# Optimization experiments

Hardware: AMD Instinct MI355X
Metric: run time of the kernel (lower is better)

## Reference

```python
import jax, jax.numpy as jnp
import numpy as np

N_CHARS = 50257
CHAR = 512
HID = 1024
LENGTH = 2048


def setup_inputs() -> dict:
    key = jax.random.key(0)
    ks = jax.random.split(key, 8)
    s = 1.0 / np.sqrt(HID)
    sh = 1.0 / np.sqrt(HID)
    return {
        "inputs": jax.random.normal(ks[0], (HID,), jnp.float32),
        "embed": (jax.random.normal(ks[1], (N_CHARS, CHAR), jnp.float32) * 0.02),
        "W_ih": jax.random.uniform(ks[2], (4 * HID, CHAR), jnp.float32, -s, s),
        "W_hh": jax.random.uniform(ks[3], (4 * HID, HID), jnp.float32, -s, s),
        "b_ih": jax.random.uniform(ks[4], (4 * HID,), jnp.float32, -s, s),
        "b_hh": jax.random.uniform(ks[5], (4 * HID,), jnp.float32, -s, s),
        "W_head": jax.random.uniform(ks[6], (N_CHARS, HID), jnp.float32, -sh, sh),
        "b_head": jax.random.uniform(ks[7], (N_CHARS,), jnp.float32, -sh, sh),
        "length": LENGTH,
        "start": 5,
    }


def _lstm_cell(x, h, c, W_ih, W_hh, b_ih, b_hh):
    # PyTorch gate order: i, f, g, o
    gates = W_ih @ x + b_ih + W_hh @ h + b_hh  # [4H]
    i, f, g, o = jnp.split(gates, 4)
    i = jax.nn.sigmoid(i)
    f = jax.nn.sigmoid(f)
    g = jnp.tanh(g)
    o = jax.nn.sigmoid(o)
    c = f * c + i * g
    h = o * jnp.tanh(c)
    return h, c


def reference(inputs, embed, W_ih, W_hh, b_ih, b_hh, W_head, b_head, length, start):
    h0 = inputs                       # latent used as initial hidden state
    c0 = jnp.zeros_like(inputs)
    x0 = embed[start]                 # [CHAR]

    def step(carry, _):
        h, c, x = carry
        h, c = _lstm_cell(x, h, c, W_ih, W_hh, b_ih, b_hh)
        logits = W_head @ h + b_head  # [N_CHARS]
        char = jnp.argmax(logits)
        x = embed[char]
        return (h, c, x), (char, logits)

    _, (chars, logits) = jax.lax.scan(step, (h0, c0, x0), None, length=length)
    return chars, logits
```

## Files before the change

### kernel.cpp

```cpp
#include <hip/hip_runtime.h>
#include <stdint.h>
#include <math.h>

#define HID   1024
#define CHARD 512
#define NC    50257
#define TLEN  2048
#define NBLK  256
#define NTHR  512
#define NGRP2 2048
#define GR    25
#define GRREG 6
#define GRLDS 19
#define NBH   1571
#define SQ    4064.0f
#define INVSQ (1.0f/4064.0f)
#define QERR  (0.5f/4064.0f)
#define CANDR 192
#define FLAGSTRIDE 16

typedef unsigned long long ull;
typedef unsigned char u8;
typedef float f32x4 __attribute__((ext_vector_type(4)));

__device__ __forceinline__ unsigned ford(float f) {
    unsigned b = __float_as_uint(f);
    return (b & 0x80000000u) ? ~b : (b | 0x80000000u);
}
__device__ __forceinline__ float unford(unsigned u) {
    return __uint_as_float((u & 0x80000000u) ? (u & 0x7FFFFFFFu) : ~u);
}
__device__ __forceinline__ ull packkv(float v, unsigned j) {
    return ((ull)ford(v) << 32) | (ull)(0xFFFFFFFFu - j);
}
__device__ __forceinline__ ull umaxu(ull a, ull b) { return a > b ? a : b; }
__device__ __forceinline__ ull shflx_ull(ull v, int m) {
    unsigned lo = (unsigned)v, hi = (unsigned)(v >> 32);
    lo = __shfl_xor(lo, m);
    hi = __shfl_xor(hi, m);
    return ((ull)hi << 32) | lo;
}

#define ALOADF(p)    __hip_atomic_load((p), __ATOMIC_RELAXED, __HIP_MEMORY_SCOPE_AGENT)
#define ASTORE(p, v) __hip_atomic_store((p), (v), __ATOMIC_RELAXED, __HIP_MEMORY_SCOPE_AGENT)

__global__ __launch_bounds__(256) void k_init(const float* __restrict__ inputs,
                                              float* __restrict__ hh,
                                              float* __restrict__ c,
                                              unsigned* __restrict__ flagarea)
{
    int g = blockIdx.x * 256 + threadIdx.x;
    if (g < HID) { hh[g] = inputs[g]; c[g] = 0.f; }
    for (int i = g; i < 2 * NBLK * FLAGSTRIDE + 16; i += 2048) flagarea[i] = 0u;
}

__global__ __launch_bounds__(256) void k_quant(const float* __restrict__ W,
                                               u8* __restrict__ W8)
{
    size_t base = ((size_t)blockIdx.x * 256 + threadIdx.x) * 16;
    if (base >= (size_t)NC * HID) return;
    const float4* src = (const float4*)(W + base);
    uint out[4];
    #pragma unroll
    for (int g = 0; g < 4; ++g) {
        float4 w = src[g];
        int a0 = (__float2int_rn(w.x * SQ) + 128) & 255;
        int a1 = (__float2int_rn(w.y * SQ) + 128) & 255;
        int a2 = (__float2int_rn(w.z * SQ) + 128) & 255;
        int a3 = (__float2int_rn(w.w * SQ) + 128) & 255;
        out[g] = (uint)(a0 | (a1 << 8) | (a2 << 16) | (a3 << 24));
    }
    *(uint4*)(W8 + base) = make_uint4(out[0], out[1], out[2], out[3]);
}

__device__ __forceinline__ float exact_logit(const float4* hs4,
                                             const float* __restrict__ W_head,
                                             const float* __restrict__ b_head,
                                             int j, int lane)
{
    const float4* wr = (const float4*)(W_head + (size_t)j * HID);
    float a = 0.f;
    #pragma unroll
    for (int m = 0; m < 4; ++m) {
        float4 w = wr[m * 64 + lane], v = hs4[m * 64 + lane];
        a = fmaf(w.x, v.x, a); a = fmaf(w.y, v.y, a);
        a = fmaf(w.z, v.z, a); a = fmaf(w.w, v.w, a);
    }
    #pragma unroll
    for (int off = 32; off > 0; off >>= 1) a += __shfl_xor(a, off);
    return a + b_head[j];
}

__device__ __forceinline__ unsigned resolve_char(const float4* hs4,
                                                 ull* bm, float* abuf,
                                                 const float* __restrict__ W_head,
                                                 const float* __restrict__ b_head,
                                                 float Sh, ull* red8, int tid)
{
    __shared__ int s_cnt, s_gcnt;
    __shared__ int s_grps[32];
    __shared__ int s_rows[CANDR];

    const int wave = tid >> 6;
    const int lane = tid & 63;

    ull bmv[4];
    ull pm = 0ull;
    #pragma unroll
    for (int rep = 0; rep < NGRP2 / NTHR; ++rep) {
        bmv[rep] = ALOADF(&bm[tid + rep * NTHR]);
        pm = umaxu(pm, bmv[rep]);
    }
    #pragma unroll
    for (int off = 32; off > 0; off >>= 1) pm = umaxu(pm, shflx_ull(pm, off));
    if (lane == 0) red8[wave] = pm;
    if (tid == 0) { s_cnt = 0; s_gcnt = 0; }
    __syncthreads();
    pm = red8[0];
    #pragma unroll
    for (int w = 1; w < 8; ++w) pm = umaxu(pm, red8[w]);
    const float mtil = unford((unsigned)(pm >> 32));
    const float E = QERR * Sh * 1.02f + 1e-4f;
    const float thresh = mtil - 2.0f * E;
    const ull pkth = ((ull)ford(thresh)) << 32;

    #pragma unroll
    for (int rep = 0; rep < NGRP2 / NTHR; ++rep) {
        if (bmv[rep] >= pkth) {
            int p = atomicAdd(&s_gcnt, 1);
            if (p < 32) s_grps[p] = tid + rep * NTHR;
        }
    }
    __syncthreads();
    const int ngr = s_gcnt;
    int ncr;
    if (ngr <= 32) {
        for (int gq = 0; gq < ngr; ++gq) {
            const int j = s_grps[gq] * GR + tid;
            if (tid < GR && j < NC) {
                float av = ALOADF(&abuf[j]);
                if (av >= thresh) {
                    int p = atomicAdd(&s_cnt, 1);
                    if (p < CANDR) s_rows[p] = j;
                }
            }
        }
        __syncthreads();
        ncr = s_cnt;
    } else {
        ncr = CANDR + 1;
    }

    ull best = 0ull;
    if (ncr <= CANDR) {
        for (int q = wave; q < ncr; q += 8) {
            const int j = s_rows[q];
            best = umaxu(best, packkv(exact_logit(hs4, W_head, b_head, j, lane),
                                      (unsigned)j));
        }
    } else {
        for (int i = wave; i < NGRP2; i += 8) {
            ull bv = ALOADF(&bm[i]);
            if (bv >= pkth) {
                const int jb = i * GR;
                const int je = jb + GR < NC ? jb + GR : NC;
                for (int j = jb; j < je; ++j) {
                    float av = ALOADF(&abuf[j]);
                    if (av >= thresh)
                        best = umaxu(best, packkv(exact_logit(hs4, W_head, b_head, j, lane),
                                                  (unsigned)j));
                }
            }
        }
    }
    __syncthreads();
    if (lane == 0) red8[wave] = best;
    __syncthreads();
    best = red8[0];
    #pragma unroll
    for (int w = 1; w < 8; ++w) best = umaxu(best, red8[w]);
    unsigned idx = 0xFFFFFFFFu - (unsigned)(best & 0xFFFFFFFFull);
    return idx < NC ? idx : (NC - 1);
}

__device__ __forceinline__ float dot16u(uint4 q, float4 h0, float4 h1,
                                        float4 h2, float4 h3)
{
    float a = 0.f;
    a = fmaf((float)(q.x & 255u), h0.x, a);
    a = fmaf((float)((q.x >> 8) & 255u), h0.y, a);
    a = fmaf((float)((q.x >> 16) & 255u), h0.z, a);
    a = fmaf((float)(q.x >> 24), h0.w, a);
    a = fmaf((float)(q.y & 255u), h1.x, a);
    a = fmaf((float)((q.y >> 8) & 255u), h1.y, a);
    a = fmaf((float)((q.y >> 16) & 255u), h1.z, a);
    a = fmaf((float)(q.y >> 24), h1.w, a);
    a = fmaf((float)(q.z & 255u), h2.x, a);
    a = fmaf((float)((q.z >> 8) & 255u), h2.y, a);
    a = fmaf((float)((q.z >> 16) & 255u), h2.z, a);
    a = fmaf((float)(q.z >> 24), h2.w, a);
    a = fmaf((float)(q.w & 255u), h3.x, a);
    a = fmaf((float)((q.w >> 8) & 255u), h3.y, a);
    a = fmaf((float)((q.w >> 16) & 255u), h3.z, a);
    a = fmaf((float)(q.w >> 24), h3.w, a);
    return a;
}

__global__ __launch_bounds__(NTHR, 1) void k_persist(
    const float* __restrict__ W_ih, const float* __restrict__ W_hh,
    const float* __restrict__ b_ih, const float* __restrict__ b_hh,
    const float* __restrict__ embed,
    const float* __restrict__ W_head, const float* __restrict__ b_head,
    const u8* __restrict__ W8,
    float* hh, float* abuf, ull* bm,
    float* __restrict__ chars_out, const int* __restrict__ startp,
    unsigned* flags, unsigned* gen)
{
    __shared__ uint4  w8L[8][GRLDS][64];
    __shared__ float4 hs4[HID / 4];
    __shared__ float4 xs4[CHARD / 4];
    __shared__ ull    red8[8];
    __shared__ float  sred[8], sred2[8];
    __shared__ int    s_brk;

    const int b    = blockIdx.x;
    const int tid  = threadIdx.x;
    const int wave = tid >> 6;
    const int lane = tid & 63;
    const int rL   = b * 4 + wave;
    const int g    = b * 8 + wave;
    const int jb   = g * GR;
    const u8* Wp   = W8 + (size_t)jb * HID;

    uint4 qb[GRREG];
    #pragma unroll
    for (int rr = 0; rr < GRREG; ++rr) {
        const int j = jb + rr;
        qb[rr] = (j < NC) ? ((const uint4*)(Wp + (size_t)rr * HID))[lane]
                          : make_uint4(0, 0, 0, 0);
    }
    #pragma unroll
    for (int rr = 0; rr < GRLDS; ++rr) {
        const int j = jb + GRREG + rr;
        w8L[wave][rr][lane] = (j < NC)
            ? ((const uint4*)(Wp + (size_t)(GRREG + rr) * HID))[lane]
            : make_uint4(0, 0, 0, 0);
    }

    float bsum[4] = {0.f, 0.f, 0.f, 0.f};
    if (wave < 4) {
        #pragma unroll
        for (int q = 0; q < 4; ++q) bsum[q] = b_ih[q * HID + rL] + b_hh[q * HID + rL];
    }
    if (tid == 0) s_brk = 0;
    float creg = 0.f;
    __syncthreads();

    float Sh;
    {
        float sa = 0.f;
        if (tid < 256) {
            float4 hv = ((const float4*)hh)[tid];
            hs4[tid] = hv;
            sa = fabsf(hv.x) + fabsf(hv.y) + fabsf(hv.z) + fabsf(hv.w);
        }
        #pragma unroll
        for (int off = 32; off > 0; off >>= 1) sa += __shfl_xor(sa, off);
        if (lane == 0) sred[wave] = sa;
        __syncthreads();
        Sh = 0.f;
        #pragma unroll
        for (int w = 0; w < 8; ++w) Sh += sred[w];
    }

    unsigned bk = 0;

    #define GRIDBAR()                                                              \
    do {                                                                           \
        ++bk;                                                                      \
        __syncthreads();                                                           \
        if (b == 0) {                                                              \
            if (!s_brk && tid > 0 && tid < NBLK) {                                 \
                int guard = 0;                                                     \
                while (__hip_atomic_load(&flags[tid * FLAGSTRIDE],                 \
                         __ATOMIC_RELAXED, __HIP_MEMORY_SCOPE_AGENT) < bk) {       \
                    __builtin_amdgcn_s_sleep(1);                                   \
                    if (++guard > (1 << 24)) { s_brk = 1; break; }                 \
                }                                                                  \
            }                                                                      \
            __syncthreads();                                                       \
            if (tid < NBLK)                                                        \
                __hip_atomic_store(&gen[tid * FLAGSTRIDE], bk, __ATOMIC_RELAXED,   \
                                   __HIP_MEMORY_SCOPE_AGENT);                      \
        } else {                                                                   \
            if (tid == 0) {                                                        \
                __hip_atomic_store(&flags[b * FLAGSTRIDE], bk, __ATOMIC_RELAXED,   \
                                   __HIP_MEMORY_SCOPE_AGENT);                      \
                if (!s_brk) {                                                      \
                    int guard = 0;                                                 \
                    while (__hip_atomic_load(&gen[b * FLAGSTRIDE],                 \
                             __ATOMIC_RELAXED, __HIP_MEMORY_SCOPE_AGENT) < bk) {   \
                        __builtin_amdgcn_s_sleep(1);                               \
                        if (++guard > (1 << 24)) { s_brk = 1; break; }             \
                    }                                                              \
                }                                                                  \
            }                                                                      \
            __syncthreads();                                                       \
        }                                                                          \
    } while (0)

    for (int t = 0; t < TLEN; ++t) {
        unsigned idx;
        if (t == 0) {
            idx = (unsigned)startp[0];
        } else {
            idx = resolve_char(hs4, bm, abuf, W_head, b_head, Sh, red8, tid);
            if (b == 0 && tid == 0) chars_out[t - 1] = (float)idx;
        }
        if (tid < 128) xs4[tid] = ((const float4*)(embed + (size_t)idx * CHARD))[tid];
        __syncthreads();

        if (wave < 4) {
            float acc[4];
            #pragma unroll
            for (int q = 0; q < 4; ++q) {
                const float4* wi = (const float4*)(W_ih + (size_t)(q * HID + rL) * CHARD);
                const float4* wh = (const float4*)(W_hh + (size_t)(q * HID + rL) * HID);
                float a = 0.f;
                #pragma unroll
                for (int m = 0; m < 2; ++m) {
                    float4 w = wi[m * 64 + lane], v = xs4[m * 64 + lane];
                    a = fmaf(w.x, v.x, a); a = fmaf(w.y, v.y, a);
                    a = fmaf(w.z, v.z, a); a = fmaf(w.w, v.w, a);
                }
                #pragma unroll
                for (int m = 0; m < 4; ++m) {
                    float4 w = wh[m * 64 + lane], v = hs4[m * 64 + lane];
                    a = fmaf(w.x, v.x, a); a = fmaf(w.y, v.y, a);
                    a = fmaf(w.z, v.z, a); a = fmaf(w.w, v.w, a);
                }
                acc[q] = a;
            }
            #pragma unroll
            for (int q = 0; q < 4; ++q) {
                #pragma unroll
                for (int off = 32; off > 0; off >>= 1) acc[q] += __shfl_xor(acc[q], off);
            }
            if (lane == 0) {
                float ig = 1.f / (1.f + expf(-(acc[0] + bsum[0])));
                float fg = 1.f / (1.f + expf(-(acc[1] + bsum[1])));
                float gg = tanhf(acc[2] + bsum[2]);
                float og = 1.f / (1.f + expf(-(acc[3] + bsum[3])));
                creg = fg * creg + ig * gg;
                ASTORE(&hh[(size_t)(t + 1) * HID + rL], og * tanhf(creg));
            }
        }

        GRIDBAR();

        {
            float sa = 0.f, ss = 0.f;
            if (tid < 256) {
                float4 hv = ((const float4*)(hh + (size_t)(t + 1) * HID))[tid];
                hs4[tid] = hv;
                sa = fabsf(hv.x) + fabsf(hv.y) + fabsf(hv.z) + fabsf(hv.w);
                ss = hv.x + hv.y + hv.z + hv.w;
            }
            #pragma unroll
            for (int off = 32; off > 0; off >>= 1) {
                sa += __shfl_xor(sa, off);
                ss += __shfl_xor(ss, off);
            }
            if (lane == 0) { sred[wave] = sa; sred2[wave] = ss; }
        }
        __syncthreads();
        float Hsum = 0.f;
        Sh = 0.f;
        #pragma unroll
        for (int w = 0; w < 8; ++w) { Sh += sred[w]; Hsum += sred2[w]; }

        const float4 H0 = hs4[lane * 4 + 0];
        const float4 H1 = hs4[lane * 4 + 1];
        const float4 H2 = hs4[lane * 4 + 2];
        const float4 H3 = hs4[lane * 4 + 3];

        ull pmw = 0ull;
        #pragma unroll
        for (int rr = 0; rr < GRREG; ++rr) {
            const int j = jb + rr;
            if (j < NC) {
                float a = dot16u(qb[rr], H0, H1, H2, H3);
                #pragma unroll
                for (int off = 32; off > 0; off >>= 1) a += __shfl_xor(a, off);
                const float v = (a - 128.f * Hsum) * INVSQ + b_head[j];
                if (lane == 0) ASTORE(&abuf[j], v);
                pmw = umaxu(pmw, packkv(v, (unsigned)j));
            }
        }
        #pragma unroll
        for (int rr = 0; rr < GRLDS; ++rr) {
            const int j = jb + GRREG + rr;
            if (j < NC) {
                float a = dot16u(w8L[wave][rr][lane], H0, H1, H2, H3);
                #pragma unroll
                for (int off = 32; off > 0; off >>= 1) a += __shfl_xor(a, off);
                const float v = (a - 128.f * Hsum) * INVSQ + b_head[j];
                if (lane == 0) ASTORE(&abuf[j], v);
                pmw = umaxu(pmw, packkv(v, (unsigned)j));
            }
        }
        if (lane == 0) ASTORE(&bm[g], pmw);

        GRIDBAR();
    }

    if (b == 0) {
        unsigned idx = resolve_char(hs4, bm, abuf, W_head, b_head, Sh, red8, tid);
        if (tid == 0) chars_out[TLEN - 1] = (float)idx;
    }
    #undef GRIDBAR
}

#define GJ 64
#define GT 128
#define GK 16
__global__ __launch_bounds__(256) void k_gemm(const float* __restrict__ W_head,
                                              const float* __restrict__ b_head,
                                              const float* __restrict__ hh,
                                              float* __restrict__ logits)
{
    __shared__ float Ws[GK][GJ + 4];
    __shared__ float Hs[GK][GT + 1];

    const int tid = threadIdx.x;
    const int j0 = blockIdx.x * GJ;
    const int t0 = blockIdx.y * GT;
    const int tj = tid & 15;
    const int tt = tid >> 4;

    const int wlj = tid >> 2;
    const int wlk = (tid & 3) * 4;
    const int hlt = tid >> 1;
    const int hlk = (tid & 1) * 8;
    const float* Wrow = W_head + (size_t)(j0 + wlj) * HID;
    const bool wvalid = (j0 + wlj) < NC;

    float acc[8][4];
    #pragma unroll
    for (int bb = 0; bb < 8; ++bb)
        #pragma unroll
        for (int a = 0; a < 4; ++a) acc[bb][a] = 0.f;

    for (int k0 = 0; k0 < HID; k0 += GK) {
        __syncthreads();
        float4 wv = wvalid ? *(const float4*)(Wrow + k0 + wlk) : make_float4(0, 0, 0, 0);
        Ws[wlk + 0][wlj] = wv.x; Ws[wlk + 1][wlj] = wv.y;
        Ws[wlk + 2][wlj] = wv.z; Ws[wlk + 3][wlj] = wv.w;
        const float* hp = hh + (size_t)(t0 + hlt + 1) * HID + k0 + hlk;
        float4 a0 = *(const float4*)hp;
        float4 a1 = *(const float4*)(hp + 4);
        Hs[hlk + 0][hlt] = a0.x; Hs[hlk + 1][hlt] = a0.y;
        Hs[hlk + 2][hlt] = a0.z; Hs[hlk + 3][hlt] = a0.w;
        Hs[hlk + 4][hlt] = a1.x; Hs[hlk + 5][hlt] = a1.y;
        Hs[hlk + 6][hlt] = a1.z; Hs[hlk + 7][hlt] = a1.w;
        __syncthreads();
        #pragma unroll
        for (int kk = 0; kk < GK; ++kk) {
            float4 w4 = *(const float4*)&Ws[kk][tj * 4];
            float hvv[8];
            #pragma unroll
            for (int bb = 0; bb < 8; ++bb) hvv[bb] = Hs[kk][tt + 16 * bb];
            #pragma unroll
            for (int bb = 0; bb < 8; ++bb) {
                acc[bb][0] = fmaf(w4.x, hvv[bb], acc[bb][0]);
                acc[bb][1] = fmaf(w4.y, hvv[bb], acc[bb][1]);
                acc[bb][2] = fmaf(w4.z, hvv[bb], acc[bb][2]);
                acc[bb][3] = fmaf(w4.w, hvv[bb], acc[bb][3]);
            }
        }
    }

    const int j = j0 + tj * 4;
    float b0 = (j + 0 < NC) ? b_head[j + 0] : 0.f;
    float b1 = (j + 1 < NC) ? b_head[j + 1] : 0.f;
    float b2 = (j + 2 < NC) ? b_head[j + 2] : 0.f;
    float b3 = (j + 3 < NC) ? b_head[j + 3] : 0.f;
    #pragma unroll
    for (int bb = 0; bb < 8; ++bb) {
        const int t = t0 + tt + 16 * bb;
        float* dst = logits + (size_t)t * NC + j;
        if (j + 3 < NC) {
            f32x4 o = { acc[bb][0] + b0, acc[bb][1] + b1,
                        acc[bb][2] + b2, acc[bb][3] + b3 };
            __builtin_nontemporal_store(o, (f32x4*)dst);
        } else {
            if (j + 0 < NC) dst[0] = acc[bb][0] + b0;
            if (j + 1 < NC) dst[1] = acc[bb][1] + b1;
            if (j + 2 < NC) dst[2] = acc[bb][2] + b2;
        }
    }
}

__global__ __launch_bounds__(256) void k_init_fb(const float* __restrict__ inputs,
                                                 const int* __restrict__ startp,
                                                 float* __restrict__ h0,
                                                 float* __restrict__ c,
                                                 ull* __restrict__ blockmax)
{
    int tid = blockIdx.x * 256 + threadIdx.x;
    if (tid < NBH) blockmax[tid] = (tid == 0) ? packkv(3.0e38f, (unsigned)startp[0]) : 0ull;
    if (tid < HID) { h0[tid] = inputs[tid]; c[tid] = 0.f; }
}

__global__ __launch_bounds__(256) void k_lstm_fb(const float* __restrict__ W_ih,
                                                 const float* __restrict__ W_hh,
                                                 const float* __restrict__ b_ih,
                                                 const float* __restrict__ b_hh,
                                                 const float* __restrict__ embed,
                                                 const ull* __restrict__ blockmax,
                                                 const float* __restrict__ h_in,
                                                 float* __restrict__ h_out,
                                                 float* __restrict__ c,
                                                 float* __restrict__ chars_out,
                                                 int t)
{
    __shared__ float4 xs4[CHARD / 4];
    __shared__ float4 hs4[HID / 4];
    __shared__ ull    red[256];
    const int tid = threadIdx.x;
    ull pm = 0ull;
    for (int i = tid; i < NBH; i += 256) pm = umaxu(pm, blockmax[i]);
    red[tid] = pm;
    __syncthreads();
    for (int s = 128; s > 0; s >>= 1) {
        if (tid < s) red[tid] = umaxu(red[tid], red[tid + s]);
        __syncthreads();
    }
    const unsigned idx = 0xFFFFFFFFu - (unsigned)(red[0] & 0xFFFFFFFFull);
    if (t > 0 && blockIdx.x == 0 && tid == 0) chars_out[t - 1] = (float)idx;
    const float4* ex = (const float4*)(embed + (size_t)idx * CHARD);
    if (tid < 128) xs4[tid] = ex[tid];
    hs4[tid] = ((const float4*)h_in)[tid];
    __syncthreads();
    const int wave = tid >> 6, lane = tid & 63;
    const int r = blockIdx.x * 4 + wave;
    float acc[4];
    #pragma unroll
    for (int q = 0; q < 4; ++q) {
        const float4* wi = (const float4*)(W_ih + (size_t)(q * HID + r) * CHARD);
        const float4* wh = (const float4*)(W_hh + (size_t)(q * HID + r) * HID);
        float a = 0.f;
        #pragma unroll
        for (int m = 0; m < 2; ++m) {
            float4 w = wi[m * 64 + lane], v = xs4[m * 64 + lane];
            a = fmaf(w.x, v.x, a); a = fmaf(w.y, v.y, a);
            a = fmaf(w.z, v.z, a); a = fmaf(w.w, v.w, a);
        }
        #pragma unroll
        for (int m = 0; m < 4; ++m) {
            float4 w = wh[m * 64 + lane], v = hs4[m * 64 + lane];
            a = fmaf(w.x, v.x, a); a = fmaf(w.y, v.y, a);
            a = fmaf(w.z, v.z, a); a = fmaf(w.w, v.w, a);
        }
        acc[q] = a;
    }
    #pragma unroll
    for (int q = 0; q < 4; ++q)
        #pragma unroll
        for (int off = 32; off > 0; off >>= 1) acc[q] += __shfl_xor(acc[q], off);
    if (lane == 0) {
        float zi = acc[0] + b_ih[r]           + b_hh[r];
        float zf = acc[1] + b_ih[HID + r]     + b_hh[HID + r];
        float zg = acc[2] + b_ih[2 * HID + r] + b_hh[2 * HID + r];
        float zo = acc[3] + b_ih[3 * HID + r] + b_hh[3 * HID + r];
        float ig = 1.f / (1.f + expf(-zi));
        float fg = 1.f / (1.f + expf(-zf));
        float gg = tanhf(zg);
        float og = 1.f / (1.f + expf(-zo));
        float cn = fg * c[r] + ig * gg;
        c[r] = cn;
        h_out[r] = og * tanhf(cn);
    }
}

__global__ __launch_bounds__(256) void k_head_fb(const float* __restrict__ W_head,
                                                 const float* __restrict__ b_head,
                                                 const float* __restrict__ h_in,
                                                 float* __restrict__ logits,
                                                 ull* __restrict__ blockmax)
{
    __shared__ float4 hs4[HID / 4];
    __shared__ ull    wmax[4];
    const int tid = threadIdx.x;
    hs4[tid] = ((const float4*)h_in)[tid];
    __syncthreads();
    const int wave = tid >> 6, lane = tid & 63;
    const int base = blockIdx.x * 32 + wave * 8;
    ull pm = 0ull;
    #pragma unroll
    for (int rep = 0; rep < 8; ++rep) {
        const int j = base + rep;
        if (j < NC) {
            const float4* w = (const float4*)(W_head + (size_t)j * HID);
            float a = 0.f;
            #pragma unroll
            for (int m = 0; m < 4; ++m) {
                float4 ww = w[m * 64 + lane], v = hs4[m * 64 + lane];
                a = fmaf(ww.x, v.x, a); a = fmaf(ww.y, v.y, a);
                a = fmaf(ww.z, v.z, a); a = fmaf(ww.w, v.w, a);
            }
            #pragma unroll
            for (int off = 32; off > 0; off >>= 1) a += __shfl_xor(a, off);
            const float v = a + b_head[j];
            if (lane == 0) __builtin_nontemporal_store(v, &logits[j]);
            pm = umaxu(pm, packkv(v, (unsigned)j));
        }
    }
    if (lane == 0) wmax[wave] = pm;
    __syncthreads();
    if (tid == 0)
        blockmax[blockIdx.x] = umaxu(umaxu(wmax[0], wmax[1]), umaxu(wmax[2], wmax[3]));
}

__global__ __launch_bounds__(256) void k_final_fb(const ull* __restrict__ blockmax,
                                                  float* __restrict__ chars_out)
{
    __shared__ ull red[256];
    const int tid = threadIdx.x;
    ull pm = 0ull;
    for (int i = tid; i < NBH; i += 256) pm = umaxu(pm, blockmax[i]);
    red[tid] = pm;
    __syncthreads();
    for (int s = 128; s > 0; s >>= 1) {
        if (tid < s) red[tid] = umaxu(red[tid], red[tid + s]);
        __syncthreads();
    }
    if (tid == 0)
        chars_out[TLEN - 1] = (float)(0xFFFFFFFFu - (unsigned)(red[0] & 0xFFFFFFFFull));
}

extern "C" void kernel_launch(void* const* d_in, const int* in_sizes, int n_in,
                              void* d_out, int out_size, void* d_ws, size_t ws_size,
                              hipStream_t stream)
{
    const float* inputs = (const float*)d_in[0];
    const float* embed  = (const float*)d_in[1];
    const float* W_ih   = (const float*)d_in[2];
    const float* W_hh   = (const float*)d_in[3];
    const float* b_ih   = (const float*)d_in[4];
    const float* b_hh   = (const float*)d_in[5];
    const float* W_head = (const float*)d_in[6];
    const float* b_head = (const float*)d_in[7];
    const int*   startp = (const int*)d_in[9];

    float* out        = (float*)d_out;
    float* chars_out  = out;
    float* logits_out = out + TLEN;

    char* ws = (char*)d_ws;
    const size_t off_hh    = 0;
    const size_t off_c     = off_hh + (size_t)(TLEN + 1) * HID * 4;
    const size_t off_ab    = off_c + (size_t)HID * 4;
    const size_t off_bm    = (off_ab + (size_t)NC * 4 + 15) & ~(size_t)15;
    const size_t off_flags = (off_bm + (size_t)NGRP2 * 8 + 63) & ~(size_t)63;
    const size_t off_w8    = (off_flags + (size_t)(2 * NBLK * FLAGSTRIDE + 16) * 4 + 15)
                             & ~(size_t)15;
    const size_t need      = off_w8 + (size_t)NC * HID;

    if (ws_size >= need) {
        float*    hh    = (float*)(ws + off_hh);
        float*    c     = (float*)(ws + off_c);
        float*    abuf  = (float*)(ws + off_ab);
        ull*      bm    = (ull*)(ws + off_bm);
        unsigned* flags = (unsigned*)(ws + off_flags);
        unsigned* gen   = flags + NBLK * FLAGSTRIDE;
        u8*       W8    = (u8*)(ws + off_w8);

        hipLaunchKernelGGL(k_init, dim3(8), dim3(256), 0, stream, inputs, hh, c, flags);
        hipLaunchKernelGGL(k_quant, dim3((NC * HID / 16 + 255) / 256), dim3(256), 0,
                           stream, W_head, W8);
        hipLaunchKernelGGL(k_persist, dim3(NBLK), dim3(NTHR), 0, stream,
                           W_ih, W_hh, b_ih, b_hh, embed, W_head, b_head, W8,
                           hh, abuf, bm, chars_out, startp, flags, gen);
        hipLaunchKernelGGL(k_gemm, dim3((NC + GJ - 1) / GJ, TLEN / GT), dim3(256), 0,
                           stream, W_head, b_head, hh, logits_out);
    } else {
        float* h0 = (float*)(ws);
        float* h1 = (float*)(ws + 4096);
        float* c  = (float*)(ws + 8192);
        ull* blockmax = (ull*)(ws + 12288);
        hipLaunchKernelGGL(k_init_fb, dim3(7), dim3(256), 0, stream,
                           inputs, startp, h0, c, blockmax);
        for (int t = 0; t < TLEN; ++t) {
            const float* hin = (t & 1) ? h1 : h0;
            float*       hout = (t & 1) ? h0 : h1;
            hipLaunchKernelGGL(k_lstm_fb, dim3(256), dim3(256), 0, stream,
                               W_ih, W_hh, b_ih, b_hh, embed, blockmax,
                               hin, hout, c, chars_out, t);
            hipLaunchKernelGGL(k_head_fb, dim3(NBH), dim3(256), 0, stream,
                               W_head, b_head, hout,
                               logits_out + (size_t)t * NC, blockmax);
        }
        hipLaunchKernelGGL(k_final_fb, dim3(1), dim3(256), 0, stream, blockmax, chars_out);
    }
}
```

Measured before the change: 46.54 ms.

## Resolve argmax candidates per group locally and use all-to-all flag grid barrier

Each wave now rescores its own group's near-max rows with exact fp32 logits right after the quantized pass. It publishes the exact best per group, so the per-step resolve becomes a plain max over group results with no candidate gathering or abuf traffic. The two-level grid barrier, where block 0 collects and then broadcasts, becomes a flat barrier: every block writes its flag and polls all flags, and the flags are packed without stride padding. This removes a serial resolve phase and a barrier hop per step. In exchange, every group performs at least one exact row dot per step, adding W_head reads, and polling on shared cache lines may cause more contention.

```diff
diff --git a/kernel.cpp b/kernel.cpp
--- a/kernel.cpp
+++ b/kernel.cpp
@@ -16,8 +16,6 @@
 #define SQ    4064.0f
 #define INVSQ (1.0f/4064.0f)
 #define QERR  (0.5f/4064.0f)
-#define CANDR 192
-#define FLAGSTRIDE 16
 
 typedef unsigned long long ull;
 typedef unsigned char u8;
@@ -47,11 +45,13 @@
 __global__ __launch_bounds__(256) void k_init(const float* __restrict__ inputs,
                                               float* __restrict__ hh,
                                               float* __restrict__ c,
-                                              unsigned* __restrict__ flagarea)
+                                              unsigned* __restrict__ flags4,
+                                              unsigned* __restrict__ bmz)
 {
     int g = blockIdx.x * 256 + threadIdx.x;
     if (g < HID) { hh[g] = inputs[g]; c[g] = 0.f; }
-    for (int i = g; i < 2 * NBLK * FLAGSTRIDE + 16; i += 2048) flagarea[i] = 0u;
+    if (g < NBLK + 16) flags4[g] = 0u;
+    for (int i = g; i < NGRP2 * 2; i += 2048) bmz[i] = 0u;
 }
 
 __global__ __launch_bounds__(256) void k_quant(const float* __restrict__ W,
@@ -91,95 +91,22 @@
     return a + b_head[j];
 }
 
-__device__ __forceinline__ unsigned resolve_char(const float4* hs4,
-                                                 ull* bm, float* abuf,
-                                                 const float* __restrict__ W_head,
-                                                 const float* __restrict__ b_head,
-                                                 float Sh, ull* red8, int tid)
-{
-    __shared__ int s_cnt, s_gcnt;
-    __shared__ int s_grps[32];
-    __shared__ int s_rows[CANDR];
-
+__device__ __forceinline__ unsigned resolve_char(ull* bm, ull* red8, int tid)
+{
     const int wave = tid >> 6;
     const int lane = tid & 63;
-
-    ull bmv[4];
     ull pm = 0ull;
     #pragma unroll
-    for (int rep = 0; rep < NGRP2 / NTHR; ++rep) {
-        bmv[rep] = ALOADF(&bm[tid + rep * NTHR]);
-        pm = umaxu(pm, bmv[rep]);
-    }
+    for (int rep = 0; rep < NGRP2 / NTHR; ++rep)
+        pm = umaxu(pm, ALOADF(&bm[tid + rep * NTHR]));
     #pragma unroll
     for (int off = 32; off > 0; off >>= 1) pm = umaxu(pm, shflx_ull(pm, off));
     if (lane == 0) red8[wave] = pm;
-    if (tid == 0) { s_cnt = 0; s_gcnt = 0; }
     __syncthreads();
     pm = red8[0];
     #pragma unroll
     for (int w = 1; w < 8; ++w) pm = umaxu(pm, red8[w]);
-    const float mtil = unford((unsigned)(pm >> 32));
-    const float E = QERR * Sh * 1.02f + 1e-4f;
-    const float thresh = mtil - 2.0f * E;
-    const ull pkth = ((ull)ford(thresh)) << 32;
-
-    #pragma unroll
-    for (int rep = 0; rep < NGRP2 / NTHR; ++rep) {
-        if (bmv[rep] >= pkth) {
-            int p = atomicAdd(&s_gcnt, 1);
-            if (p < 32) s_grps[p] = tid + rep * NTHR;
-        }
-    }
-    __syncthreads();
-    const int ngr = s_gcnt;
-    int ncr;
-    if (ngr <= 32) {
-        for (int gq = 0; gq < ngr; ++gq) {
-            const int j = s_grps[gq] * GR + tid;
-            if (tid < GR && j < NC) {
-                float av = ALOADF(&abuf[j]);
-                if (av >= thresh) {
-                    int p = atomicAdd(&s_cnt, 1);
-                    if (p < CANDR) s_rows[p] = j;
-                }
-            }
-        }
-        __syncthreads();
-        ncr = s_cnt;
-    } else {
-        ncr = CANDR + 1;
-    }
-
-    ull best = 0ull;
-    if (ncr <= CANDR) {
-        for (int q = wave; q < ncr; q += 8) {
-            const int j = s_rows[q];
-            best = umaxu(best, packkv(exact_logit(hs4, W_head, b_head, j, lane),
-                                      (unsigned)j));
-        }
-    } else {
-        for (int i = wave; i < NGRP2; i += 8) {
-            ull bv = ALOADF(&bm[i]);
-            if (bv >= pkth) {
-                const int jb = i * GR;
-                const int je = jb + GR < NC ? jb + GR : NC;
-                for (int j = jb; j < je; ++j) {
-                    float av = ALOADF(&abuf[j]);
-                    if (av >= thresh)
-                        best = umaxu(best, packkv(exact_logit(hs4, W_head, b_head, j, lane),
-                                                  (unsigned)j));
-                }
-            }
-        }
-    }
-    __syncthreads();
-    if (lane == 0) red8[wave] = best;
-    __syncthreads();
-    best = red8[0];
-    #pragma unroll
-    for (int w = 1; w < 8; ++w) best = umaxu(best, red8[w]);
-    unsigned idx = 0xFFFFFFFFu - (unsigned)(best & 0xFFFFFFFFull);
+    unsigned idx = 0xFFFFFFFFu - (unsigned)(pm & 0xFFFFFFFFull);
     return idx < NC ? idx : (NC - 1);
 }
 
@@ -212,16 +139,15 @@
     const float* __restrict__ embed,
     const float* __restrict__ W_head, const float* __restrict__ b_head,
     const u8* __restrict__ W8,
-    float* hh, float* abuf, ull* bm,
+    float* hh, ull* bm,
     float* __restrict__ chars_out, const int* __restrict__ startp,
-    unsigned* flags, unsigned* gen)
+    unsigned* flags4)
 {
     __shared__ uint4  w8L[8][GRLDS][64];
     __shared__ float4 hs4[HID / 4];
     __shared__ float4 xs4[CHARD / 4];
     __shared__ ull    red8[8];
     __shared__ float  sred[8], sred2[8];
-    __shared__ int    s_brk;
 
     const int b    = blockIdx.x;
     const int tid  = threadIdx.x;
@@ -252,26 +178,11 @@
         #pragma unroll
         for (int q = 0; q < 4; ++q) bsum[q] = b_ih[q * HID + rL] + b_hh[q * HID + rL];
     }
-    if (tid == 0) s_brk = 0;
     float creg = 0.f;
     __syncthreads();
 
-    float Sh;
-    {
-        float sa = 0.f;
-        if (tid < 256) {
-            float4 hv = ((const float4*)hh)[tid];
-            hs4[tid] = hv;
-            sa = fabsf(hv.x) + fabsf(hv.y) + fabsf(hv.z) + fabsf(hv.w);
-        }
-        #pragma unroll
-        for (int off = 32; off > 0; off >>= 1) sa += __shfl_xor(sa, off);
-        if (lane == 0) sred[wave] = sa;
-        __syncthreads();
-        Sh = 0.f;
-        #pragma unroll
-        for (int w = 0; w < 8; ++w) Sh += sred[w];
-    }
+    if (tid < 256) hs4[tid] = ((const float4*)hh)[tid];
+    __syncthreads();
 
     unsigned bk = 0;
 
@@ -279,34 +190,18 @@
     do {                                                                           \
         ++bk;                                                                      \
         __syncthreads();                                                           \
-        if (b == 0) {                                                              \
-            if (!s_brk && tid > 0 && tid < NBLK) {                                 \
-                int guard = 0;                                                     \
-                while (__hip_atomic_load(&flags[tid * FLAGSTRIDE],                 \
-                         __ATOMIC_RELAXED, __HIP_MEMORY_SCOPE_AGENT) < bk) {       \
-                    __builtin_amdgcn_s_sleep(1);                                   \
-                    if (++guard > (1 << 24)) { s_brk = 1; break; }                 \
-                }                                                                  \
+        if (tid == 0)                                                              \
+            __hip_atomic_store(&flags4[b], bk, __ATOMIC_RELAXED,                   \
+                               __HIP_MEMORY_SCOPE_AGENT);                          \
+        if (tid < NBLK) {                                                          \
+            int guard = 0;                                                         \
+            while (__hip_atomic_load(&flags4[tid], __ATOMIC_RELAXED,               \
+                                     __HIP_MEMORY_SCOPE_AGENT) < bk) {             \
+                __builtin_amdgcn_s_sleep(1);                                       \
+                if (++guard > (1 << 24)) break;                                    \
             }                                                                      \
-            __syncthreads();                                                       \
-            if (tid < NBLK)                                                        \
-                __hip_atomic_store(&gen[tid * FLAGSTRIDE], bk, __ATOMIC_RELAXED,   \
-                                   __HIP_MEMORY_SCOPE_AGENT);                      \
-        } else {                                                                   \
-            if (tid == 0) {                                                        \
-                __hip_atomic_store(&flags[b * FLAGSTRIDE], bk, __ATOMIC_RELAXED,   \
-                                   __HIP_MEMORY_SCOPE_AGENT);                      \
-                if (!s_brk) {                                                      \
-                    int guard = 0;                                                 \
-                    while (__hip_atomic_load(&gen[b * FLAGSTRIDE],                 \
-                             __ATOMIC_RELAXED, __HIP_MEMORY_SCOPE_AGENT) < bk) {   \
-                        __builtin_amdgcn_s_sleep(1);                               \
-                        if (++guard > (1 << 24)) { s_brk = 1; break; }             \
-                    }                                                              \
-                }                                                                  \
-            }                                                                      \
-            __syncthreads();                                                       \
         }                                                                          \
+        __syncthreads();                                                           \
     } while (0)
 
     for (int t = 0; t < TLEN; ++t) {
@@ -314,7 +209,7 @@
         if (t == 0) {
             idx = (unsigned)startp[0];
         } else {
-            idx = resolve_char(hs4, bm, abuf, W_head, b_head, Sh, red8, tid);
+            idx = resolve_char(bm, red8, tid);
             if (b == 0 && tid == 0) chars_out[t - 1] = (float)idx;
         }
         if (tid < 128) xs4[tid] = ((const float4*)(embed + (size_t)idx * CHARD))[tid];
@@ -374,8 +269,7 @@
             if (lane == 0) { sred[wave] = sa; sred2[wave] = ss; }
         }
         __syncthreads();
-        float Hsum = 0.f;
-        Sh = 0.f;
+        float Hsum = 0.f, Sh = 0.f;
         #pragma unroll
         for (int w = 0; w < 8; ++w) { Sh += sred[w]; Hsum += sred2[w]; }
 
@@ -384,38 +278,53 @@
         const float4 H2 = hs4[lane * 4 + 2];
         const float4 H3 = hs4[lane * 4 + 3];
 
-        ull pmw = 0ull;
-        #pragma unroll
-        for (int rr = 0; rr < GRREG; ++rr) {
-            const int j = jb + rr;
-            if (j < NC) {
-                float a = dot16u(qb[rr], H0, H1, H2, H3);
-                #pragma unroll
-                for (int off = 32; off > 0; off >>= 1) a += __shfl_xor(a, off);
-                const float v = (a - 128.f * Hsum) * INVSQ + b_head[j];
-                if (lane == 0) ASTORE(&abuf[j], v);
-                pmw = umaxu(pmw, packkv(v, (unsigned)j));
-            }
-        }
-        #pragma unroll
-        for (int rr = 0; rr < GRLDS; ++rr) {
-            const int j = jb + GRREG + rr;
-            if (j < NC) {
-                float a = dot16u(w8L[wave][rr][lane], H0, H1, H2, H3);
-                #pragma unroll
-                for (int off = 32; off > 0; off >>= 1) a += __shfl_xor(a, off);
-                const float v = (a - 128.f * Hsum) * INVSQ + b_head[j];
-                if (lane == 0) ASTORE(&abuf[j], v);
-                pmw = umaxu(pmw, packkv(v, (unsigned)j));
-            }
-        }
-        if (lane == 0) ASTORE(&bm[g], pmw);
+        if (jb < NC) {
+            ull pmw = 0ull;
+            float sv = -3.0e38f;
+            #pragma unroll
+            for (int rr = 0; rr < GRREG; ++rr) {
+                const int j = jb + rr;
+                if (j < NC) {
+                    float a = dot16u(qb[rr], H0, H1, H2, H3);
+                    #pragma unroll
+                    for (int off = 32; off > 0; off >>= 1) a += __shfl_xor(a, off);
+                    const float v = (a - 128.f * Hsum) * INVSQ + b_head[j];
+                    if (lane == rr) sv = v;
+                    pmw = umaxu(pmw, packkv(v, (unsigned)j));
+                }
+            }
+            #pragma unroll
+            for (int rr = 0; rr < GRLDS; ++rr) {
+                const int j = jb + GRREG + rr;
+                if (j < NC) {
+                    float a = dot16u(w8L[wave][rr][lane], H0, H1, H2, H3);
+                    #pragma unroll
+                    for (int off = 32; off > 0; off >>= 1) a += __shfl_xor(a, off);
+                    const float v = (a - 128.f * Hsum) * INVSQ + b_head[j];
+                    if (lane == GRREG + rr) sv = v;
+                    pmw = umaxu(pmw, packkv(v, (unsigned)j));
+                }
+            }
+            const float stv = unford((unsigned)(pmw >> 32));
+            const float E   = QERR * Sh * 1.02f + 1e-4f;
+            const float thr = stv - 2.0f * E;
+            ull cand = __ballot(lane < GR && (jb + lane) < NC && sv >= thr);
+            ull beste = 0ull;
+            while (cand) {
+                const int s = __builtin_ctzll(cand);
+                cand &= cand - 1;
+                const int j = jb + s;
+                const float ev = exact_logit(hs4, W_head, b_head, j, lane);
+                beste = umaxu(beste, packkv(ev, (unsigned)j));
+            }
+            if (lane == 0) ASTORE(&bm[g], beste);
+        }
 
         GRIDBAR();
     }
 
     if (b == 0) {
-        unsigned idx = resolve_char(hs4, bm, abuf, W_head, b_head, Sh, red8, tid);
+        unsigned idx = resolve_char(bm, red8, tid);
         if (tid == 0) chars_out[TLEN - 1] = (float)idx;
     }
     #undef GRIDBAR
@@ -660,28 +569,25 @@
     char* ws = (char*)d_ws;
     const size_t off_hh    = 0;
     const size_t off_c     = off_hh + (size_t)(TLEN + 1) * HID * 4;
-    const size_t off_ab    = off_c + (size_t)HID * 4;
-    const size_t off_bm    = (off_ab + (size_t)NC * 4 + 15) & ~(size_t)15;
+    const size_t off_bm    = (off_c + (size_t)HID * 4 + 15) & ~(size_t)15;
     const size_t off_flags = (off_bm + (size_t)NGRP2 * 8 + 63) & ~(size_t)63;
-    const size_t off_w8    = (off_flags + (size_t)(2 * NBLK * FLAGSTRIDE + 16) * 4 + 15)
-                             & ~(size_t)15;
+    const size_t off_w8    = (off_flags + (size_t)(NBLK + 16) * 4 + 15) & ~(size_t)15;
     const size_t need      = off_w8 + (size_t)NC * HID;
 
     if (ws_size >= need) {
-        float*    hh    = (float*)(ws + off_hh);
-        float*    c     = (float*)(ws + off_c);
-        float*    abuf  = (float*)(ws + off_ab);
-        ull*      bm    = (ull*)(ws + off_bm);
-        unsigned* flags = (unsigned*)(ws + off_flags);
-        unsigned* gen   = flags + NBLK * FLAGSTRIDE;
-        u8*       W8    = (u8*)(ws + off_w8);
-
-        hipLaunchKernelGGL(k_init, dim3(8), dim3(256), 0, stream, inputs, hh, c, flags);
+        float*    hh     = (float*)(ws + off_hh);
+        float*    c      = (float*)(ws + off_c);
+        ull*      bm     = (ull*)(ws + off_bm);
+        unsigned* flags4 = (unsigned*)(ws + off_flags);
+        u8*       W8     = (u8*)(ws + off_w8);
+
+        hipLaunchKernelGGL(k_init, dim3(8), dim3(256), 0, stream,
+                           inputs, hh, c, flags4, (unsigned*)bm);
         hipLaunchKernelGGL(k_quant, dim3((NC * HID / 16 + 255) / 256), dim3(256), 0,
                            stream, W_head, W8);
         hipLaunchKernelGGL(k_persist, dim3(NBLK), dim3(NTHR), 0, stream,
                            W_ih, W_hh, b_ih, b_hh, embed, W_head, b_head, W8,
-                           hh, abuf, bm, chars_out, startp, flags, gen);
+                           hh, bm, chars_out, startp, flags4);
         hipLaunchKernelGGL(k_gemm, dim3((NC + GJ - 1) / GJ, TLEN / GT), dim3(256), 0,
                            stream, W_head, b_head, hh, logits_out);
     } else {
```

New measurement: 61.19 ms. +31.5%, slower.

## Replace master-driven grid barrier with all-to-all flags and fused top-2 argmax exchange

Applied to the files above, without the earlier changes.

Replaces the two-phase grid barrier, where block 0 gathers per-block flags and broadcasts a generation, with a flat barrier in which every block polls all 256 packed flags. The second barrier per step now carries each block's top-1 and runner-up quantized logits, so every block can reduce the global top-2 itself. When the margin exceeds the quantization error bound, the character is taken directly, skipping the bm scan and candidate resolution that ran each step. In exchange, every block polls every flag, which adds memory traffic, and the index is packed into 16 bits.

```diff
diff --git a/kernel.cpp b/kernel.cpp
--- a/kernel.cpp
+++ b/kernel.cpp
@@ -17,7 +17,6 @@
 #define INVSQ (1.0f/4064.0f)
 #define QERR  (0.5f/4064.0f)
 #define CANDR 192
-#define FLAGSTRIDE 16
 
 typedef unsigned long long ull;
 typedef unsigned char u8;
@@ -47,11 +46,16 @@
 __global__ __launch_bounds__(256) void k_init(const float* __restrict__ inputs,
                                               float* __restrict__ hh,
                                               float* __restrict__ c,
-                                              unsigned* __restrict__ flagarea)
+                                              unsigned* __restrict__ flags4,
+                                              ull* __restrict__ recA,
+                                              ull* __restrict__ recB,
+                                              ull* __restrict__ bm)
 {
     int g = blockIdx.x * 256 + threadIdx.x;
     if (g < HID) { hh[g] = inputs[g]; c[g] = 0.f; }
-    for (int i = g; i < 2 * NBLK * FLAGSTRIDE + 16; i += 2048) flagarea[i] = 0u;
+    if (g < NBLK + 16) flags4[g] = 0u;
+    if (g < NBLK) { recA[g] = 0ull; recB[g] = 0ull; }
+    if (g < NGRP2) bm[g] = 0ull;
 }
 
 __global__ __launch_bounds__(256) void k_quant(const float* __restrict__ W,
@@ -91,44 +95,26 @@
     return a + b_head[j];
 }
 
-__device__ __forceinline__ unsigned resolve_char(const float4* hs4,
-                                                 ull* bm, float* abuf,
-                                                 const float* __restrict__ W_head,
-                                                 const float* __restrict__ b_head,
-                                                 float Sh, ull* red8, int tid)
+__device__ unsigned resolve_fb(const float4* hs4, ull* bm, float* abuf,
+                               const float* __restrict__ W_head,
+                               const float* __restrict__ b_head,
+                               float mtil, float E, ull* red8, int tid)
 {
     __shared__ int s_cnt, s_gcnt;
     __shared__ int s_grps[32];
     __shared__ int s_rows[CANDR];
-
     const int wave = tid >> 6;
     const int lane = tid & 63;
-
-    ull bmv[4];
-    ull pm = 0ull;
-    #pragma unroll
-    for (int rep = 0; rep < NGRP2 / NTHR; ++rep) {
-        bmv[rep] = ALOADF(&bm[tid + rep * NTHR]);
-        pm = umaxu(pm, bmv[rep]);
-    }
-    #pragma unroll
-    for (int off = 32; off > 0; off >>= 1) pm = umaxu(pm, shflx_ull(pm, off));
-    if (lane == 0) red8[wave] = pm;
-    if (tid == 0) { s_cnt = 0; s_gcnt = 0; }
-    __syncthreads();
-    pm = red8[0];
-    #pragma unroll
-    for (int w = 1; w < 8; ++w) pm = umaxu(pm, red8[w]);
-    const float mtil = unford((unsigned)(pm >> 32));
-    const float E = QERR * Sh * 1.02f + 1e-4f;
     const float thresh = mtil - 2.0f * E;
     const ull pkth = ((ull)ford(thresh)) << 32;
-
+    if (tid == 0) { s_cnt = 0; s_gcnt = 0; }
+    __syncthreads();
     #pragma unroll
     for (int rep = 0; rep < NGRP2 / NTHR; ++rep) {
-        if (bmv[rep] >= pkth) {
+        const int i = tid + rep * NTHR;
+        if (ALOADF(&bm[i]) >= pkth) {
             int p = atomicAdd(&s_gcnt, 1);
-            if (p < 32) s_grps[p] = tid + rep * NTHR;
+            if (p < 32) s_grps[p] = i;
         }
     }
     __syncthreads();
@@ -138,8 +124,7 @@
         for (int gq = 0; gq < ngr; ++gq) {
             const int j = s_grps[gq] * GR + tid;
             if (tid < GR && j < NC) {
-                float av = ALOADF(&abuf[j]);
-                if (av >= thresh) {
+                if (ALOADF(&abuf[j]) >= thresh) {
                     int p = atomicAdd(&s_cnt, 1);
                     if (p < CANDR) s_rows[p] = j;
                 }
@@ -147,9 +132,7 @@
         }
         __syncthreads();
         ncr = s_cnt;
-    } else {
-        ncr = CANDR + 1;
-    }
+    } else ncr = CANDR + 1;
 
     ull best = 0ull;
     if (ncr <= CANDR) {
@@ -160,16 +143,13 @@
         }
     } else {
         for (int i = wave; i < NGRP2; i += 8) {
-            ull bv = ALOADF(&bm[i]);
-            if (bv >= pkth) {
-                const int jb = i * GR;
-                const int je = jb + GR < NC ? jb + GR : NC;
-                for (int j = jb; j < je; ++j) {
-                    float av = ALOADF(&abuf[j]);
-                    if (av >= thresh)
+            if (ALOADF(&bm[i]) >= pkth) {
+                const int jb2 = i * GR;
+                const int je = jb2 + GR < NC ? jb2 + GR : NC;
+                for (int j = jb2; j < je; ++j)
+                    if (ALOADF(&abuf[j]) >= thresh)
                         best = umaxu(best, packkv(exact_logit(hs4, W_head, b_head, j, lane),
                                                   (unsigned)j));
-                }
             }
         }
     }
@@ -214,14 +194,15 @@
     const u8* __restrict__ W8,
     float* hh, float* abuf, ull* bm,
     float* __restrict__ chars_out, const int* __restrict__ startp,
-    unsigned* flags, unsigned* gen)
+    unsigned* flags4, ull* recA, ull* recB)
 {
     __shared__ uint4  w8L[8][GRLDS][64];
     __shared__ float4 hs4[HID / 4];
     __shared__ float4 xs4[CHARD / 4];
     __shared__ ull    red8[8];
     __shared__ float  sred[8], sred2[8];
-    __shared__ int    s_brk;
+    __shared__ ull    wtop[8], gt8[8];
+    __shared__ float  wsec[8], gs8[8];
 
     const int b    = blockIdx.x;
     const int tid  = threadIdx.x;
@@ -252,7 +233,6 @@
         #pragma unroll
         for (int q = 0; q < 4; ++q) bsum[q] = b_ih[q * HID + rL] + b_hh[q * HID + rL];
     }
-    if (tid == 0) s_brk = 0;
     float creg = 0.f;
     __syncthreads();
 
@@ -274,47 +254,23 @@
     }
 
     unsigned bk = 0;
-
-    #define GRIDBAR()                                                              \
-    do {                                                                           \
-        ++bk;                                                                      \
-        __syncthreads();                                                           \
-        if (b == 0) {                                                              \
-            if (!s_brk && tid > 0 && tid < NBLK) {                                 \
-                int guard = 0;                                                     \
-                while (__hip_atomic_load(&flags[tid * FLAGSTRIDE],                 \
-                         __ATOMIC_RELAXED, __HIP_MEMORY_SCOPE_AGENT) < bk) {       \
-                    __builtin_amdgcn_s_sleep(1);                                   \
-                    if (++guard > (1 << 24)) { s_brk = 1; break; }                 \
-                }                                                                  \
-            }                                                                      \
-            __syncthreads();                                                       \
-            if (tid < NBLK)                                                        \
-                __hip_atomic_store(&gen[tid * FLAGSTRIDE], bk, __ATOMIC_RELAXED,   \
-                                   __HIP_MEMORY_SCOPE_AGENT);                      \
-        } else {                                                                   \
-            if (tid == 0) {                                                        \
-                __hip_atomic_store(&flags[b * FLAGSTRIDE], bk, __ATOMIC_RELAXED,   \
-                                   __HIP_MEMORY_SCOPE_AGENT);                      \
-                if (!s_brk) {                                                      \
-                    int guard = 0;                                                 \
-                    while (__hip_atomic_load(&gen[b * FLAGSTRIDE],                 \
-                             __ATOMIC_RELAXED, __HIP_MEMORY_SCOPE_AGENT) < bk) {   \
-                        __builtin_amdgcn_s_sleep(1);                               \
-                        if (++guard > (1 << 24)) { s_brk = 1; break; }             \
-                    }                                                              \
-                }                                                                  \
-            }                                                                      \
-            __syncthreads();                                                       \
-        }                                                                          \
-    } while (0)
+    ull   g_top = 0ull;
+    float g_sec = -3.0e38f;
 
     for (int t = 0; t < TLEN; ++t) {
         unsigned idx;
         if (t == 0) {
             idx = (unsigned)startp[0];
         } else {
-            idx = resolve_char(hs4, bm, abuf, W_head, b_head, Sh, red8, tid);
+            const float gv = unford((unsigned)(g_top >> 32));
+            unsigned gidx = 0xFFFFu - ((unsigned)(g_top >> 16) & 0xFFFFu);
+            if (gidx >= NC) gidx = NC - 1;
+            const float E = QERR * Sh * 1.02f + 1e-4f;
+            if (gv - 2.0f * E > g_sec) {
+                idx = gidx;
+            } else {
+                idx = resolve_fb(hs4, bm, abuf, W_head, b_head, gv, E, red8, tid);
+            }
             if (b == 0 && tid == 0) chars_out[t - 1] = (float)idx;
         }
         if (tid < 128) xs4[tid] = ((const float4*)(embed + (size_t)idx * CHARD))[tid];
@@ -356,7 +312,18 @@
             }
         }
 
-        GRIDBAR();
+        ++bk;
+        __syncthreads();
+        if (tid == 0)
+            ASTORE(&flags4[b], bk);
+        if (tid < NBLK) {
+            int guard = 0;
+            while (ALOADF(&flags4[tid]) < bk) {
+                __builtin_amdgcn_s_sleep(1);
+                if (++guard > (1 << 24)) break;
+            }
+        }
+        __syncthreads();
 
         {
             float sa = 0.f, ss = 0.f;
@@ -385,40 +352,130 @@
         const float4 H3 = hs4[lane * 4 + 3];
 
         ull pmw = 0ull;
-        #pragma unroll
-        for (int rr = 0; rr < GRREG; ++rr) {
-            const int j = jb + rr;
-            if (j < NC) {
-                float a = dot16u(qb[rr], H0, H1, H2, H3);
-                #pragma unroll
-                for (int off = 32; off > 0; off >>= 1) a += __shfl_xor(a, off);
-                const float v = (a - 128.f * Hsum) * INVSQ + b_head[j];
-                if (lane == 0) ASTORE(&abuf[j], v);
-                pmw = umaxu(pmw, packkv(v, (unsigned)j));
-            }
-        }
-        #pragma unroll
-        for (int rr = 0; rr < GRLDS; ++rr) {
-            const int j = jb + GRREG + rr;
-            if (j < NC) {
-                float a = dot16u(w8L[wave][rr][lane], H0, H1, H2, H3);
-                #pragma unroll
-                for (int off = 32; off > 0; off >>= 1) a += __shfl_xor(a, off);
-                const float v = (a - 128.f * Hsum) * INVSQ + b_head[j];
-                if (lane == 0) ASTORE(&abuf[j], v);
-                pmw = umaxu(pmw, packkv(v, (unsigned)j));
-            }
-        }
-        if (lane == 0) ASTORE(&bm[g], pmw);
-
-        GRIDBAR();
+        float gsec = -3.0e38f;
+        if (jb < NC) {
+            float sv = -3.0e38f;
+            #pragma unroll
+            for (int rr = 0; rr < GRREG; ++rr) {
+                const int j = jb + rr;
+                if (j < NC) {
+                    float a = dot16u(qb[rr], H0, H1, H2, H3);
+                    #pragma unroll
+                    for (int off = 32; off > 0; off >>= 1) a += __shfl_xor(a, off);
+                    const float v = (a - 128.f * Hsum) * INVSQ + b_head[j];
+                    if (lane == rr) sv = v;
+                    if (lane == 0) ASTORE(&abuf[j], v);
+                    pmw = umaxu(pmw, packkv(v, (unsigned)j));
+                }
+            }
+            #pragma unroll
+            for (int rr = 0; rr < GRLDS; ++rr) {
+                const int j = jb + GRREG + rr;
+                if (j < NC) {
+                    float a = dot16u(w8L[wave][rr][lane], H0, H1, H2, H3);
+                    #pragma unroll
+                    for (int off = 32; off > 0; off >>= 1) a += __shfl_xor(a, off);
+                    const float v = (a - 128.f * Hsum) * INVSQ + b_head[j];
+                    if (lane == GRREG + rr) sv = v;
+                    if (lane == 0) ASTORE(&abuf[j], v);
+                    pmw = umaxu(pmw, packkv(v, (unsigned)j));
+                }
+            }
+            const int stop = (int)(0xFFFFFFFFu - (unsigned)(pmw & 0xFFFFFFFFull)) - jb;
+            float s2 = (lane == stop) ? -3.0e38f : sv;
+            #pragma unroll
+            for (int off = 32; off > 0; off >>= 1) s2 = fmaxf(s2, __shfl_xor(s2, off));
+            gsec = s2;
+            if (lane == 0) ASTORE(&bm[g], pmw);
+        }
+        if (lane == 0) { wtop[wave] = pmw; wsec[wave] = gsec; }
+
+        ++bk;
+        __syncthreads();
+        {
+            ull bt = 0ull; float bs = -3.0e38f;
+            #pragma unroll
+            for (int w = 0; w < 8; ++w) {
+                ull tt = wtop[w]; float ssv = wsec[w];
+                bs = fmaxf(bs, ssv);
+                if (tt) {
+                    if (bt) {
+                        ull lo = bt < tt ? bt : tt;
+                        bs = fmaxf(bs, unford((unsigned)(lo >> 32)));
+                        bt = bt > tt ? bt : tt;
+                    } else bt = tt;
+                }
+            }
+            if (tid == 0) {
+                ull ra;
+                if (bt) {
+                    unsigned idx32 = 0xFFFFFFFFu - (unsigned)(bt & 0xFFFFFFFFull);
+                    unsigned inv16 = 0xFFFFu - (idx32 & 0xFFFFu);
+                    ra = ((bt >> 32) << 32) | ((ull)inv16 << 16) | (ull)(bk & 0xFFFFu);
+                } else {
+                    ra = (ull)(bk & 0xFFFFu);
+                }
+                ASTORE(&recA[b], ra);
+                ull rb = (((ull)ford(bs)) << 16) | (ull)(bk & 0xFFFFu);
+                ASTORE(&recB[b], rb);
+            }
+            ull mt = 0ull; float msv = -3.0e38f;
+            if (tid < NBLK) {
+                ull rA = 0ull, rB = 0ull;
+                int guard = 0;
+                for (;;) {
+                    rA = ALOADF(&recA[tid]);
+                    rB = ALOADF(&recB[tid]);
+                    if (((rA ^ (ull)bk) & 0xFFFFull) == 0 &&
+                        ((rB ^ (ull)bk) & 0xFFFFull) == 0) break;
+                    __builtin_amdgcn_s_sleep(1);
+                    if (++guard > (1 << 24)) break;
+                }
+                if (rA >> 32) mt = rA & ~0xFFFFull;
+                msv = unford((unsigned)(rB >> 16));
+            }
+            #pragma unroll
+            for (int off = 32; off > 0; off >>= 1) {
+                ull pt = shflx_ull(mt, off);
+                float ps = __shfl_xor(msv, off);
+                msv = fmaxf(msv, ps);
+                if (pt) {
+                    if (mt) {
+                        ull lo = mt < pt ? mt : pt;
+                        msv = fmaxf(msv, unford((unsigned)(lo >> 32)));
+                        mt = mt > pt ? mt : pt;
+                    } else mt = pt;
+                }
+            }
+            if (lane == 0) { gt8[wave] = mt; gs8[wave] = msv; }
+            __syncthreads();
+            mt = 0ull; msv = -3.0e38f;
+            #pragma unroll
+            for (int w = 0; w < 8; ++w) {
+                ull tt = gt8[w]; float ssv = gs8[w];
+                msv = fmaxf(msv, ssv);
+                if (tt) {
+                    if (mt) {
+                        ull lo = mt < tt ? mt : tt;
+                        msv = fmaxf(msv, unford((unsigned)(lo >> 32)));
+                        mt = mt > tt ? mt : tt;
+                    } else mt = tt;
+                }
+            }
+            g_top = mt;
+            g_sec = msv;
+        }
     }
 
     if (b == 0) {
-        unsigned idx = resolve_char(hs4, bm, abuf, W_head, b_head, Sh, red8, tid);
+        const float gv = unford((unsigned)(g_top >> 32));
+        unsigned gidx = 0xFFFFu - ((unsigned)(g_top >> 16) & 0xFFFFu);
+        if (gidx >= NC) gidx = NC - 1;
+        const float E = QERR * Sh * 1.02f + 1e-4f;
+        unsigned idx = (gv - 2.0f * E > g_sec) ? gidx
+                     : resolve_fb(hs4, bm, abuf, W_head, b_head, gv, E, red8, tid);
         if (tid == 0) chars_out[TLEN - 1] = (float)idx;
     }
-    #undef GRIDBAR
 }
 
 #define GJ 64
@@ -662,26 +719,29 @@
     const size_t off_c     = off_hh + (size_t)(TLEN + 1) * HID * 4;
     const size_t off_ab    = off_c + (size_t)HID * 4;
     const size_t off_bm    = (off_ab + (size_t)NC * 4 + 15) & ~(size_t)15;
-    const size_t off_flags = (off_bm + (size_t)NGRP2 * 8 + 63) & ~(size_t)63;
-    const size_t off_w8    = (off_flags + (size_t)(2 * NBLK * FLAGSTRIDE + 16) * 4 + 15)
-                             & ~(size_t)15;
+    const size_t off_fl    = (off_bm + (size_t)NGRP2 * 8 + 63) & ~(size_t)63;
+    const size_t off_ra    = (off_fl + (size_t)(NBLK + 16) * 4 + 63) & ~(size_t)63;
+    const size_t off_rb    = off_ra + (size_t)NBLK * 8;
+    const size_t off_w8    = (off_rb + (size_t)NBLK * 8 + 15) & ~(size_t)15;
     const size_t need      = off_w8 + (size_t)NC * HID;
 
     if (ws_size >= need) {
-        float*    hh    = (float*)(ws + off_hh);
-        float*    c     = (float*)(ws + off_c);
-        float*    abuf  = (float*)(ws + off_ab);
-        ull*      bm    = (ull*)(ws + off_bm);
-        unsigned* flags = (unsigned*)(ws + off_flags);
-        unsigned* gen   = flags + NBLK * FLAGSTRIDE;
-        u8*       W8    = (u8*)(ws + off_w8);
-
-        hipLaunchKernelGGL(k_init, dim3(8), dim3(256), 0, stream, inputs, hh, c, flags);
+        float*    hh     = (float*)(ws + off_hh);
+        float*    c      = (float*)(ws + off_c);
+        float*    abuf   = (float*)(ws + off_ab);
+        ull*      bm     = (ull*)(ws + off_bm);
+        unsigned* flags4 = (unsigned*)(ws + off_fl);
+        ull*      recA   = (ull*)(ws + off_ra);
+        ull*      recB   = (ull*)(ws + off_rb);
+        u8*       W8     = (u8*)(ws + off_w8);
+
+        hipLaunchKernelGGL(k_init, dim3(8), dim3(256), 0, stream,
+                           inputs, hh, c, flags4, recA, recB, bm);
         hipLaunchKernelGGL(k_quant, dim3((NC * HID / 16 + 255) / 256), dim3(256), 0,
                            stream, W_head, W8);
         hipLaunchKernelGGL(k_persist, dim3(NBLK), dim3(NTHR), 0, stream,
                            W_ih, W_hh, b_ih, b_hh, embed, W_head, b_head, W8,
-                           hh, abuf, bm, chars_out, startp, flags, gen);
+                           hh, abuf, bm, chars_out, startp, flags4, recA, recB);
         hipLaunchKernelGGL(k_gemm, dim3((NC + GJ - 1) / GJ, TLEN / GT), dim3(256), 0,
                            stream, W_head, b_head, hh, logits_out);
     } else {
```

Result: slower. 89.94 ms (+93.3%).
